# Kernel tuning notes

Measured on AMD Instinct MI355X. Metric: run time of the kernel, lower is better.

## Reference

```python
import jax, jax.numpy as jnp
import numpy as np

NB, D, ED, N, K, DTR = 4, 1024, 2048, 32, 4, 64
B, L = 1, 1024


def setup_inputs():
    key = jax.random.key(0)
    ks = jax.random.split(key, 10)
    g = lambda k, s, sc=0.02: jax.random.normal(k, s, dtype=jnp.float32) * sc
    A_log = jnp.log(jnp.broadcast_to(jnp.arange(1, N + 1, dtype=jnp.float32), (NB, ED, N))) + 0.0
    return {
        "x": g(ks[0], (B, L, D), 1.0),
        "Wi": g(ks[1], (D, D)),
        "bi": jnp.zeros((D,), jnp.float32),
        "ln_g": jnp.ones((NB, D), jnp.float32),
        "ln_b": jnp.zeros((NB, D), jnp.float32),
        "in_w": g(ks[2], (NB, 2 * ED, D)),
        "conv_w": g(ks[3], (NB, ED, 1, K), 0.2),
        "conv_b": jnp.zeros((NB, ED), jnp.float32),
        "xproj_w": g(ks[4], (NB, DTR + 2 * N, ED)),
        "dtproj_w": g(ks[5], (NB, ED, DTR), 0.1),
        "dtproj_b": jnp.full((NB, ED), -4.0, jnp.float32),
        "A_log": A_log,
        "Dp": jnp.ones((NB, ED), jnp.float32),
        "out_w": g(ks[6], (NB, D, ED)),
        "fn_g": jnp.ones((D,), jnp.float32),
        "fn_b": jnp.zeros((D,), jnp.float32),
        "sp_w": g(ks[7], (N, D)),
        "sp_b": jnp.zeros((N,), jnp.float32),
    }


def layernorm(x, g, b, eps=1e-5):
    m = jnp.mean(x, axis=-1, keepdims=True)
    v = jnp.mean(jnp.square(x - m), axis=-1, keepdims=True)
    return (x - m) * jax.lax.rsqrt(v + eps) * g + b


def mamba(u_in, in_w, conv_w, conv_b, xproj_w, dtproj_w, dtproj_b, A_log, Dp, out_w):
    # u_in: (B, L, D)
    xz = u_in @ in_w.T                       # (B, L, 2*ED)
    u, z = jnp.split(xz, 2, axis=-1)         # each (B, L, ED)
    # causal depthwise conv over time
    uc = jnp.swapaxes(u, 1, 2)               # (B, ED, L)
    uc = jax.lax.conv_general_dilated(uc, conv_w, (1,), [(K - 1, 0)], feature_group_count=ED)
    uc = uc + conv_b[None, :, None]
    u = jax.nn.silu(jnp.swapaxes(uc, 1, 2))  # (B, L, ED)
    x_dbl = u @ xproj_w.T                    # (B, L, DTR + 2N)
    dt, Bm, Cm = jnp.split(x_dbl, [DTR, DTR + N], axis=-1)
    delta = jax.nn.softplus(dt @ dtproj_w.T + dtproj_b)  # (B, L, ED)
    A = -jnp.exp(A_log)                                  # (ED, N)
    dA = jnp.exp(delta[..., None] * A)                   # (B, L, ED, N)
    dBu = (delta * u)[..., None] * Bm[:, :, None, :]     # (B, L, ED, N)

    def step(h, inp):
        dA_t, dBu_t, C_t = inp
        h = dA_t * h + dBu_t
        y = jnp.einsum('ben,bn->be', h, C_t)
        return h, y

    h0 = jnp.zeros((u.shape[0], ED, N), u.dtype)
    _, ys = jax.lax.scan(step, h0, (jnp.swapaxes(dA, 0, 1), jnp.swapaxes(dBu, 0, 1), jnp.swapaxes(Cm, 0, 1)))
    y = jnp.swapaxes(ys, 0, 1) + u * Dp      # (B, L, ED)
    y = y * jax.nn.silu(z)
    return y @ out_w.T                       # (B, L, D)


def reference(x, Wi, bi, ln_g, ln_b, in_w, conv_w, conv_b, xproj_w, dtproj_w, dtproj_b, A_log, Dp, out_w, fn_g, fn_b, sp_w, sp_b):
    h = x @ Wi.T + bi
    for i in range(NB):
        normed = layernorm(h, ln_g[i], ln_b[i])
        h = h + mamba(normed, in_w[i], conv_w[i], conv_b[i], xproj_w[i],
                      dtproj_w[i], dtproj_b[i], A_log[i], Dp[i], out_w[i])
    h = layernorm(h, fn_g, fn_b)
    state = jnp.mean(h, axis=1) @ sp_w.T + sp_b   # (B, N)
    return h, state
```

## Files before the change

kernel.cpp:

```cpp
#include <hip/hip_runtime.h>
#include <math.h>

#define D_    1024
#define ED_   2048
#define NST   32
#define KCONV 4
#define DTR_  64
#define L_    1024
#define NB_   4
#define NCH   8
#define CHUNK (L_ / NCH)
#define ZSPL  4
#define XPZ   16

typedef __bf16 bf16_8 __attribute__((ext_vector_type(8)));
typedef __bf16 bf16_4 __attribute__((ext_vector_type(4)));
typedef float  f32x4  __attribute__((ext_vector_type(4)));

__device__ __forceinline__ float softplus_f(float x) {
  return x > 20.f ? x : log1pf(expf(x));
}
__device__ __forceinline__ float silu_f(float x) {
  return x / (1.f + expf(-x));
}

__device__ __forceinline__ int xcd_swz(int lin, int nwg) {
  const int q = nwg >> 3;
  return (lin & 7) * q + (lin >> 3);
}

__global__ __launch_bounds__(256) void f2bf4_k(
    const float* __restrict__ i0, __bf16* __restrict__ o0, int n0,
    const float* __restrict__ i1, __bf16* __restrict__ o1, int n1,
    const float* __restrict__ i2, __bf16* __restrict__ o2, int n2,
    const float* __restrict__ i3, __bf16* __restrict__ o3, int n3)
{
  int gid = blockIdx.x * 256 + threadIdx.x;
  const int u0 = n0 >> 3, u1 = n1 >> 3, u2 = n2 >> 3, u3 = n3 >> 3;
  const float* in; __bf16* out;
  if (gid < u0) { in = i0; out = o0; }
  else if ((gid -= u0) < u1) { in = i1; out = o1; }
  else if ((gid -= u1) < u2) { in = i2; out = o2; }
  else if ((gid -= u2) < u3) { in = i3; out = o3; }
  else return;
  const int i = gid * 8;
  const float4 a = *reinterpret_cast<const float4*>(in + i);
  const float4 b = *reinterpret_cast<const float4*>(in + i + 4);
  bf16_8 v;
  v[0]=(__bf16)a.x; v[1]=(__bf16)a.y; v[2]=(__bf16)a.z; v[3]=(__bf16)a.w;
  v[4]=(__bf16)b.x; v[5]=(__bf16)b.y; v[6]=(__bf16)b.z; v[7]=(__bf16)b.w;
  *reinterpret_cast<bf16_8*>(out + i) = v;
}

__global__ __launch_bounds__(256) void gemm_mfma(
    const __bf16* __restrict__ A, int lda,
    const __bf16* __restrict__ W, int ldw,
    const float* __restrict__ bias, float* __restrict__ C, int ldc,
    int K, int flags)
{
  __shared__ __bf16 As[128 * 64];
  __shared__ __bf16 Ws[128 * 64];
  const int tid  = threadIdx.x;
  const int lane = tid & 63;
  const int w    = tid >> 6;
  const int wr   = w >> 1, wc = w & 1;
  const int nwg  = gridDim.x * gridDim.y;
  const int swz  = xcd_swz(blockIdx.y * gridDim.x + blockIdx.x, nwg);
  const int bx   = swz % gridDim.x, by = swz / gridDim.x;
  const int row0 = by * 128, col0 = bx * 128;

  f32x4 acc[4][4] = {};

  for (int k0 = 0; k0 < K; k0 += 64) {
    #pragma unroll
    for (int j = 0; j < 4; ++j) {
      const int inst = w * 4 + j;
      const int row  = inst * 8 + (lane >> 3);
      const int lu   = (lane & 7) ^ (row & 7);
      __builtin_amdgcn_global_load_lds(
          (const __attribute__((address_space(1))) void*)(A + (size_t)(row0 + row) * lda + k0 + lu * 8),
          (__attribute__((address_space(3))) void*)(&As[inst * 512]), 16, 0, 0);
      __builtin_amdgcn_global_load_lds(
          (const __attribute__((address_space(1))) void*)(W + (size_t)(col0 + row) * ldw + k0 + lu * 8),
          (__attribute__((address_space(3))) void*)(&Ws[inst * 512]), 16, 0, 0);
    }
    __syncthreads();
    const int r16 = lane & 15;
    const int uq  = lane >> 4;
    #pragma unroll
    for (int ks = 0; ks < 2; ++ks) {
      bf16_8 af[4], bfr[4];
      #pragma unroll
      for (int m = 0; m < 4; ++m) {
        const int row = wr * 64 + m * 16 + r16;
        const int pu  = (ks * 4 + uq) ^ (row & 7);
        af[m] = *reinterpret_cast<const bf16_8*>(&As[row * 64 + pu * 8]);
      }
      #pragma unroll
      for (int n = 0; n < 4; ++n) {
        const int row = wc * 64 + n * 16 + r16;
        const int pu  = (ks * 4 + uq) ^ (row & 7);
        bfr[n] = *reinterpret_cast<const bf16_8*>(&Ws[row * 64 + pu * 8]);
      }
      #pragma unroll
      for (int m = 0; m < 4; ++m)
        #pragma unroll
        for (int n = 0; n < 4; ++n)
          acc[m][n] = __builtin_amdgcn_mfma_f32_16x16x32_bf16(af[m], bfr[n], acc[m][n], 0, 0, 0);
    }
    __syncthreads();
  }

  const int crow = (lane >> 4) * 4;
  const int ccol = lane & 15;
  #pragma unroll
  for (int m = 0; m < 4; ++m)
    #pragma unroll
    for (int n = 0; n < 4; ++n) {
      const int col = col0 + wc * 64 + n * 16 + ccol;
      const float bv = (flags & 4) ? bias[col] : 0.f;
      #pragma unroll
      for (int r = 0; r < 4; ++r) {
        const int row = row0 + wr * 64 + m * 16 + crow + r;
        float* cp = C + (size_t)row * ldc + col;
        float v = acc[m][n][r] + bv;
        if (flags & 2) v = softplus_f(v);
        if (flags & 1) v += *cp;
        *cp = v;
      }
    }
}

__global__ __launch_bounds__(256) void gemm_mfma_sk(
    const __bf16* __restrict__ A, const __bf16* __restrict__ W,
    float* __restrict__ partials, int M, int N, int K, int Kc)
{
  __shared__ __bf16 As[128 * 64];
  __shared__ __bf16 Ws[128 * 64];
  const int tid  = threadIdx.x;
  const int lane = tid & 63;
  const int w    = tid >> 6;
  const int wr   = w >> 1, wc = w & 1;
  const int nwg  = gridDim.x * gridDim.y * gridDim.z;
  const int lin  = (blockIdx.z * gridDim.y + blockIdx.y) * gridDim.x + blockIdx.x;
  const int swz  = xcd_swz(lin, nwg);
  const int bx   = swz % gridDim.x;
  const int tmp  = swz / gridDim.x;
  const int by   = tmp % gridDim.y, bz = tmp / gridDim.y;
  const int row0 = by * 128, col0 = bx * 128;
  const int kbase = bz * Kc;

  f32x4 acc[4][4] = {};

  for (int k0 = kbase; k0 < kbase + Kc; k0 += 64) {
    #pragma unroll
    for (int j = 0; j < 4; ++j) {
      const int inst = w * 4 + j;
      const int row  = inst * 8 + (lane >> 3);
      const int lu   = (lane & 7) ^ (row & 7);
      __builtin_amdgcn_global_load_lds(
          (const __attribute__((address_space(1))) void*)(A + (size_t)(row0 + row) * K + k0 + lu * 8),
          (__attribute__((address_space(3))) void*)(&As[inst * 512]), 16, 0, 0);
      __builtin_amdgcn_global_load_lds(
          (const __attribute__((address_space(1))) void*)(W + (size_t)(col0 + row) * K + k0 + lu * 8),
          (__attribute__((address_space(3))) void*)(&Ws[inst * 512]), 16, 0, 0);
    }
    __syncthreads();
    const int r16 = lane & 15;
    const int uq  = lane >> 4;
    #pragma unroll
    for (int ks = 0; ks < 2; ++ks) {
      bf16_8 af[4], bfr[4];
      #pragma unroll
      for (int m = 0; m < 4; ++m) {
        const int row = wr * 64 + m * 16 + r16;
        const int pu  = (ks * 4 + uq) ^ (row & 7);
        af[m] = *reinterpret_cast<const bf16_8*>(&As[row * 64 + pu * 8]);
      }
      #pragma unroll
      for (int n = 0; n < 4; ++n) {
        const int row = wc * 64 + n * 16 + r16;
        const int pu  = (ks * 4 + uq) ^ (row & 7);
        bfr[n] = *reinterpret_cast<const bf16_8*>(&Ws[row * 64 + pu * 8]);
      }
      #pragma unroll
      for (int m = 0; m < 4; ++m)
        #pragma unroll
        for (int n = 0; n < 4; ++n)
          acc[m][n] = __builtin_amdgcn_mfma_f32_16x16x32_bf16(af[m], bfr[n], acc[m][n], 0, 0, 0);
    }
    __syncthreads();
  }

  float* base = partials + (size_t)bz * M * N;
  const int crow = (lane >> 4) * 4;
  const int ccol = lane & 15;
  #pragma unroll
  for (int m = 0; m < 4; ++m)
    #pragma unroll
    for (int n = 0; n < 4; ++n) {
      const int col = col0 + wc * 64 + n * 16 + ccol;
      #pragma unroll
      for (int r = 0; r < 4; ++r) {
        const int row = row0 + wr * 64 + m * 16 + crow + r;
        base[(size_t)row * N + col] = acc[m][n][r];
      }
    }
}

__global__ __launch_bounds__(256) void mfma_sk_reduce(
    const float* __restrict__ partials, const float* __restrict__ bias,
    float* __restrict__ C, __bf16* __restrict__ Cbf,
    int elems, int ncols, int nz, int flags)
{
  const int i = (blockIdx.x * 256 + threadIdx.x) * 4;
  if (i >= elems) return;
  float4 s = *reinterpret_cast<const float4*>(partials + i);
  for (int z = 1; z < nz; ++z) {
    const float4 p = *reinterpret_cast<const float4*>(partials + (size_t)z * elems + i);
    s.x += p.x; s.y += p.y; s.z += p.z; s.w += p.w;
  }
  if (flags & 4) {
    const float4 bv = *reinterpret_cast<const float4*>(bias + (i % ncols));
    s.x += bv.x; s.y += bv.y; s.z += bv.z; s.w += bv.w;
  }
  if (flags & 1) {
    const float4 ov = *reinterpret_cast<const float4*>(C + i);
    s.x += ov.x; s.y += ov.y; s.z += ov.z; s.w += ov.w;
  }
  *reinterpret_cast<float4*>(C + i) = s;
  if (flags & 8) {
    bf16_4 b;
    b[0]=(__bf16)s.x; b[1]=(__bf16)s.y; b[2]=(__bf16)s.z; b[3]=(__bf16)s.w;
    *reinterpret_cast<bf16_4*>(Cbf + i) = b;
  }
}

__global__ __launch_bounds__(256) void reduce_ln_k(
    const float* __restrict__ partials, const float* __restrict__ bias,
    float* __restrict__ hbuf, const float* __restrict__ g,
    const float* __restrict__ b, __bf16* __restrict__ outbf, int flags)
{
  __shared__ float red[8];
  const int row = blockIdx.x;
  const int tid = threadIdx.x;
  const int c = tid * 4;
  const size_t off = (size_t)row * D_ + c;
  float4 v = *reinterpret_cast<const float4*>(partials + off);
  #pragma unroll
  for (int z = 1; z < ZSPL; ++z) {
    const float4 p = *reinterpret_cast<const float4*>(partials + (size_t)z * (L_*D_) + off);
    v.x += p.x; v.y += p.y; v.z += p.z; v.w += p.w;
  }
  if (flags & 4) {
    const float4 bv = *reinterpret_cast<const float4*>(bias + c);
    v.x += bv.x; v.y += bv.y; v.z += bv.z; v.w += bv.w;
  }
  if (flags & 1) {
    const float4 ov = *reinterpret_cast<const float4*>(hbuf + off);
    v.x += ov.x; v.y += ov.y; v.z += ov.z; v.w += ov.w;
  }
  *reinterpret_cast<float4*>(hbuf + off) = v;

  float s = v.x + v.y + v.z + v.w;
  #pragma unroll
  for (int o = 32; o; o >>= 1) s += __shfl_down(s, o, 64);
  if ((tid & 63) == 0) red[tid >> 6] = s;
  __syncthreads();
  const float m = (red[0] + red[1] + red[2] + red[3]) * (1.f / D_);
  float dx0 = v.x - m, dx1 = v.y - m, dx2 = v.z - m, dx3 = v.w - m;
  float ss = dx0*dx0 + dx1*dx1 + dx2*dx2 + dx3*dx3;
  #pragma unroll
  for (int o = 32; o; o >>= 1) ss += __shfl_down(ss, o, 64);
  if ((tid & 63) == 0) red[4 + (tid >> 6)] = ss;
  __syncthreads();
  const float var = (red[4] + red[5] + red[6] + red[7]) * (1.f / D_);
  const float rs = rsqrtf(var + 1e-5f);
  const float4 gv = *reinterpret_cast<const float4*>(g + c);
  const float4 bv = *reinterpret_cast<const float4*>(b + c);
  bf16_4 o;
  o[0] = (__bf16)(dx0 * rs * gv.x + bv.x);
  o[1] = (__bf16)(dx1 * rs * gv.y + bv.y);
  o[2] = (__bf16)(dx2 * rs * gv.z + bv.z);
  o[3] = (__bf16)(dx3 * rs * gv.w + bv.w);
  *reinterpret_cast<bf16_4*>(outbf + off) = o;
}

__global__ __launch_bounds__(256) void layernorm_k(
    const float* __restrict__ x, const float* __restrict__ g,
    const float* __restrict__ b, float* __restrict__ out)
{
  __shared__ float red[8];
  const int row = blockIdx.x;
  const int tid = threadIdx.x;
  const float* xr = x + (size_t)row * D_;
  float4 v = *reinterpret_cast<const float4*>(xr + tid * 4);
  float s = v.x + v.y + v.z + v.w;
  #pragma unroll
  for (int off = 32; off; off >>= 1) s += __shfl_down(s, off, 64);
  if ((tid & 63) == 0) red[tid >> 6] = s;
  __syncthreads();
  const float m = (red[0] + red[1] + red[2] + red[3]) * (1.f / D_);
  float dx0 = v.x - m, dx1 = v.y - m, dx2 = v.z - m, dx3 = v.w - m;
  float ss = dx0*dx0 + dx1*dx1 + dx2*dx2 + dx3*dx3;
  #pragma unroll
  for (int off = 32; off; off >>= 1) ss += __shfl_down(ss, off, 64);
  if ((tid & 63) == 0) red[4 + (tid >> 6)] = ss;
  __syncthreads();
  const float var = (red[4] + red[5] + red[6] + red[7]) * (1.f / D_);
  const float rs = rsqrtf(var + 1e-5f);
  const int c = tid * 4;
  const float4 gv = *reinterpret_cast<const float4*>(g + c);
  const float4 bv = *reinterpret_cast<const float4*>(b + c);
  float4 o;
  o.x = dx0 * rs * gv.x + bv.x;
  o.y = dx1 * rs * gv.y + bv.y;
  o.z = dx2 * rs * gv.z + bv.z;
  o.w = dx3 * rs * gv.w + bv.w;
  *reinterpret_cast<float4*>(out + (size_t)row * D_ + c) = o;
}

__global__ __launch_bounds__(256) void conv_silu_k(
    const float* __restrict__ xz, const float* __restrict__ cw,
    const float* __restrict__ cb, float* __restrict__ u, __bf16* __restrict__ ub)
{
  const int e = blockIdx.x * 256 + threadIdx.x;
  const int t0 = blockIdx.y * 8;
  const float w0 = cw[e*4+0], w1 = cw[e*4+1], w2 = cw[e*4+2], w3 = cw[e*4+3];
  const float b = cb[e];
  float x0 = (t0 >= 3) ? xz[(size_t)(t0-3)*(2*ED_)+e] : 0.f;
  float x1 = (t0 >= 2) ? xz[(size_t)(t0-2)*(2*ED_)+e] : 0.f;
  float x2 = (t0 >= 1) ? xz[(size_t)(t0-1)*(2*ED_)+e] : 0.f;
  #pragma unroll
  for (int j = 0; j < 8; ++j) {
    const float x3 = xz[(size_t)(t0+j)*(2*ED_)+e];
    const float uv = silu_f(b + w0*x0 + w1*x1 + w2*x2 + w3*x3);
    u[(size_t)(t0+j)*ED_+e] = uv;
    ub[(size_t)(t0+j)*ED_+e] = (__bf16)uv;
    x0 = x1; x1 = x2; x2 = x3;
  }
}

__global__ __launch_bounds__(512) void scan_phase1(
    const float* __restrict__ delta, const float* __restrict__ u,
    const float* __restrict__ xdbl, const float* __restrict__ A_log,
    float* __restrict__ hend, float* __restrict__ Pend)
{
  __shared__ float dl[32][16], ul[32][16];
  __shared__ float bl[32][36];
  const int tid = threadIdx.x;
  const int n = tid & 31;
  const int c = tid >> 5;
  const int e0 = blockIdx.x * 16;
  const int e = e0 + c;
  const int ch = blockIdx.y;
  const float a = -expf(A_log[e * NST + n]);
  float h = 0.f, S = 0.f;
  const int t0 = ch * CHUNK;
  const int s_t = tid >> 4, s_e = tid & 15;
  const int b_t = tid >> 3, b_c = (tid & 7) * 4;

  float rg_d, rg_u;
  float4 rg_b;
  rg_d = delta[(size_t)(t0 + s_t) * ED_ + e0 + s_e];
  rg_u = u[(size_t)(t0 + s_t) * ED_ + e0 + s_e];
  if (tid < 256)
    rg_b = *reinterpret_cast<const float4*>(&xdbl[(size_t)(t0 + b_t) * 128 + 64 + b_c]);

  for (int tb = 0; tb < CHUNK; tb += 32) {
    dl[s_t][s_e] = rg_d;
    ul[s_t][s_e] = rg_u;
    if (tid < 256) *reinterpret_cast<float4*>(&bl[b_t][b_c]) = rg_b;
    __syncthreads();
    if (tb + 32 < CHUNK) {
      const int t = t0 + tb + 32 + s_t;
      rg_d = delta[(size_t)t * ED_ + e0 + s_e];
      rg_u = u[(size_t)t * ED_ + e0 + s_e];
      if (tid < 256)
        rg_b = *reinterpret_cast<const float4*>(&xdbl[(size_t)(t0 + tb + 32 + b_t) * 128 + 64 + b_c]);
    }
    #pragma unroll
    for (int jp = 0; jp < 16; ++jp) {
      const float sd1 = dl[2*jp][c],   uv1 = ul[2*jp][c],   B1 = bl[2*jp][n];
      const float sd2 = dl[2*jp+1][c], uv2 = ul[2*jp+1][c], B2 = bl[2*jp+1][n];
      const float dA1 = __expf(sd1 * a);
      const float dA2 = __expf(sd2 * a);
      const float b1 = sd1 * uv1 * B1;
      const float b2 = sd2 * uv2 * B2;
      h = fmaf(dA1 * dA2, h, fmaf(dA2, b1, b2));
      S += sd1 + sd2;
    }
    __syncthreads();
  }
  const int idx = ch * (ED_ * NST) + blockIdx.x * 512 + tid;
  hend[idx] = h;
  Pend[idx] = __expf(a * S);
}

__global__ __launch_bounds__(512) void scan_phase3(
    const float* __restrict__ delta, const float* __restrict__ u,
    const float* __restrict__ xdbl, const float* __restrict__ A_log,
    const float* __restrict__ hend, const float* __restrict__ Pend,
    const float* __restrict__ Dp,
    const float* __restrict__ xz, __bf16* __restrict__ y)
{
  __shared__ __bf16 p_lds[16][16][34];
  __shared__ float dl[16][16], ul[16][16], zl[16][16];
  __shared__ float bc[16][68];
  const int tid = threadIdx.x;
  const int n = tid & 31;
  const int c = tid >> 5;
  const int e0 = blockIdx.x * 16;
  const int e = e0 + c;
  const int ch = blockIdx.y;
  const float a = -expf(A_log[e * NST + n]);
  const float dp = Dp[e];

  float h = 0.f;
  {
    const int sidx = blockIdx.x * 512 + tid;
    for (int cc = 0; cc < ch; ++cc) {
      const int off = cc * (ED_ * NST) + sidx;
      h = fmaf(Pend[off], h, hend[off]);
    }
  }

  const int t0 = ch * CHUNK;
  const int r = n & 15, half = n >> 4;
  const int s_t  = (tid & 255) >> 4;
  const int s_e  = tid & 15;
  const int bidx = tid - 256;
  const int b_t  = (bidx & 255) >> 4;
  const int b_c  = (bidx & 15) * 4;

  float rg_a = 0.f, rg_z = 0.f;
  float4 rg_bc;
  {
    const int t = t0 + s_t;
    if (tid < 256) {
      rg_a = delta[(size_t)t * ED_ + e0 + s_e];
      rg_z = xz[(size_t)t * (2*ED_) + ED_ + e0 + s_e];
    } else {
      rg_a = u[(size_t)t * ED_ + e0 + s_e];
      rg_bc = *reinterpret_cast<const float4*>(&xdbl[(size_t)(t0 + b_t) * 128 + 64 + b_c]);
    }
  }

  for (int tb = 0; tb < CHUNK; tb += 16) {
    if (tid < 256) {
      dl[s_t][s_e] = rg_a; zl[s_t][s_e] = rg_z;
    } else {
      ul[s_t][s_e] = rg_a;
      *reinterpret_cast<float4*>(&bc[b_t][b_c]) = rg_bc;
    }
    __syncthreads();
    if (tb + 16 < CHUNK) {
      const int t = t0 + tb + 16 + s_t;
      if (tid < 256) {
        rg_a = delta[(size_t)t * ED_ + e0 + s_e];
        rg_z = xz[(size_t)t * (2*ED_) + ED_ + e0 + s_e];
      } else {
        rg_a = u[(size_t)t * ED_ + e0 + s_e];
        rg_bc = *reinterpret_cast<const float4*>(&xdbl[(size_t)(t0 + tb + 16 + b_t) * 128 + 64 + b_c]);
      }
    }
    #pragma unroll
    for (int jp = 0; jp < 8; ++jp) {
      const float sd1 = dl[2*jp][c],   uv1 = ul[2*jp][c];
      const float sd2 = dl[2*jp+1][c], uv2 = ul[2*jp+1][c];
      const float B1 = bc[2*jp][n],   C1 = bc[2*jp][32 + n];
      const float B2 = bc[2*jp+1][n], C2 = bc[2*jp+1][32 + n];
      const float dA1 = __expf(sd1 * a);
      const float dA2 = __expf(sd2 * a);
      const float b1 = sd1 * uv1 * B1;
      const float b2 = sd2 * uv2 * B2;
      const float h1 = fmaf(dA1, h, b1);
      p_lds[c][2*jp][n] = (__bf16)(h1 * C1);
      h = fmaf(dA1 * dA2, h, fmaf(dA2, b1, b2));
      p_lds[c][2*jp+1][n] = (__bf16)(h * C2);
    }
    __syncthreads();
    float s = 0.f;
    #pragma unroll
    for (int k = 0; k < 8; ++k) {
      const unsigned v = *reinterpret_cast<const unsigned*>(&p_lds[c][r][half * 16 + 2 * k]);
      s += __uint_as_float(v << 16) + __uint_as_float(v & 0xffff0000u);
    }
    s += __shfl_xor(s, 16, 64);
    if (half == 0) {
      const float uvt = ul[r][c];
      const float zv  = zl[r][c];
      y[(size_t)(t0 + tb + r) * ED_ + e] = (__bf16)((s + uvt * dp) * silu_f(zv));
    }
    __syncthreads();
  }
}

__global__ __launch_bounds__(256) void colmean_part_k(
    const float* __restrict__ hf, float* __restrict__ part)
{
  const int d = blockIdx.x * 256 + threadIdx.x;
  const int tc = blockIdx.y;
  float s = 0.f;
  #pragma unroll 8
  for (int j = 0; j < 32; ++j) s += hf[(size_t)(tc * 32 + j) * D_ + d];
  part[tc * D_ + d] = s;
}

__global__ __launch_bounds__(256) void state_fused_k(
    const float* __restrict__ part, const float* __restrict__ spw,
    const float* __restrict__ spb, float* __restrict__ out)
{
  __shared__ float red[4];
  const int nidx = blockIdx.x;
  const int tid = threadIdx.x;
  float s = 0.f;
  for (int d = tid; d < D_; d += 256) {
    float cm = 0.f;
    #pragma unroll
    for (int c = 0; c < 32; ++c) cm += part[c * D_ + d];
    s += cm * (1.f / L_) * spw[(size_t)nidx * D_ + d];
  }
  #pragma unroll
  for (int off = 32; off; off >>= 1) s += __shfl_down(s, off, 64);
  if ((tid & 63) == 0) red[tid >> 6] = s;
  __syncthreads();
  if (tid == 0) out[nidx] = red[0] + red[1] + red[2] + red[3] + spb[nidx];
}

extern "C" void kernel_launch(void* const* d_in, const int* in_sizes, int n_in,
                              void* d_out, int out_size, void* d_ws, size_t ws_size,
                              hipStream_t stream) {
  const float* x        = (const float*)d_in[0];
  const float* Wi       = (const float*)d_in[1];
  const float* bi       = (const float*)d_in[2];
  const float* ln_g     = (const float*)d_in[3];
  const float* ln_b     = (const float*)d_in[4];
  const float* in_w     = (const float*)d_in[5];
  const float* conv_w   = (const float*)d_in[6];
  const float* conv_b   = (const float*)d_in[7];
  const float* xproj_w  = (const float*)d_in[8];
  const float* dtproj_w = (const float*)d_in[9];
  const float* dtproj_b = (const float*)d_in[10];
  const float* A_log    = (const float*)d_in[11];
  const float* Dp       = (const float*)d_in[12];
  const float* out_w    = (const float*)d_in[13];
  const float* fn_g     = (const float*)d_in[14];
  const float* fn_b     = (const float*)d_in[15];
  const float* sp_w     = (const float*)d_in[16];
  const float* sp_b     = (const float*)d_in[17];
  float* out  = (float*)d_out;
  float* ws_f = (float*)d_ws;

  float* h_buf  = ws_f;
  float* xz     = ws_f + 1048576;
  float* u_buf  = ws_f + 5242880;
  float* xdbl   = ws_f + 7340032;
  float* delta  = ws_f + 7471104;
  float* hend   = ws_f + 9568256;
  float* pend   = ws_f + 10092544;
  __bf16* nbf   = (__bf16*)(ws_f + 10617856);
  __bf16* ybf   = (__bf16*)(ws_f + 11142144);
  __bf16* wbf   = (__bf16*)(ws_f + 12190720);
  __bf16* xdblbf= (__bf16*)(ws_f + 16385024);
  __bf16* dtwbf = (__bf16*)(ws_f + 16450560);
  __bf16* ubf   = (__bf16*)(ws_f + 16516096);
  __bf16* xpbf  = (__bf16*)(ws_f + 17564672);
  __bf16* owbf  = (__bf16*)(ws_f + 17695744);
  float* skmf   = u_buf;
  float* skxp   = delta;
  float* cmpart = hend;

  const dim3 blk(256);
  const dim3 blk512(512);

  f2bf4_k<<<1024, blk, 0, stream>>>(x, nbf, L_*D_, Wi, wbf, D_*D_,
                                    x, nbf, 0, x, nbf, 0);
  gemm_mfma_sk<<<dim3(D_/128, L_/128, ZSPL), blk, 0, stream>>>(
      nbf, wbf, skmf, L_, D_, D_, D_/ZSPL);
  reduce_ln_k<<<L_, blk, 0, stream>>>(
      skmf, bi, h_buf, ln_g, ln_b, nbf, 4);

  for (int i = 0; i < NB_; ++i) {
    f2bf4_k<<<3264, blk, 0, stream>>>(
        in_w    + (size_t)i*2*ED_*D_, wbf,   2*ED_*D_,
        xproj_w + (size_t)i*128*ED_,  xpbf,  128*ED_,
        dtproj_w+ (size_t)i*ED_*DTR_, dtwbf, ED_*DTR_,
        out_w   + (size_t)i*D_*ED_,   owbf,  D_*ED_);
    gemm_mfma<<<dim3(2*ED_/128, L_/128), blk, 0, stream>>>(
        nbf, D_, wbf, D_, nullptr, xz, 2*ED_, D_, 0);
    conv_silu_k<<<dim3(ED_/256, L_/8), blk, 0, stream>>>(
        xz, conv_w + (size_t)i*ED_*KCONV, conv_b + (size_t)i*ED_, u_buf, ubf);
    gemm_mfma_sk<<<dim3(1, L_/128, XPZ), blk, 0, stream>>>(
        ubf, xpbf, skxp, L_, 128, ED_, ED_/XPZ);
    mfma_sk_reduce<<<dim3(L_*128/4/256), blk, 0, stream>>>(
        skxp, nullptr, xdbl, xdblbf, L_*128, 128, XPZ, 8);
    gemm_mfma<<<dim3(ED_/128, L_/128), blk, 0, stream>>>(
        xdblbf, 128, dtwbf, DTR_, dtproj_b + (size_t)i*ED_, delta, ED_, DTR_, 2 | 4);
    scan_phase1<<<dim3(ED_/16, NCH), blk512, 0, stream>>>(
        delta, u_buf, xdbl, A_log + (size_t)i*ED_*NST, hend, pend);
    scan_phase3<<<dim3(ED_/16, NCH), blk512, 0, stream>>>(
        delta, u_buf, xdbl, A_log + (size_t)i*ED_*NST, hend, pend,
        Dp + (size_t)i*ED_, xz, ybf);
    gemm_mfma_sk<<<dim3(D_/128, L_/128, ZSPL), blk, 0, stream>>>(
        ybf, owbf, skmf, L_, D_, ED_, ED_/ZSPL);
    if (i < NB_ - 1) {
      reduce_ln_k<<<L_, blk, 0, stream>>>(
          skmf, nullptr, h_buf, ln_g + (i+1)*D_, ln_b + (i+1)*D_, nbf, 1);
    } else {
      mfma_sk_reduce<<<dim3(L_*D_/4/256), blk, 0, stream>>>(
          skmf, nullptr, h_buf, nullptr, L_*D_, D_, ZSPL, 1);
    }
  }

  layernorm_k<<<L_, blk, 0, stream>>>(h_buf, fn_g, fn_b, out);
  colmean_part_k<<<dim3(D_/256, 32), blk, 0, stream>>>(out, cmpart);
  state_fused_k<<<NST, blk, 0, stream>>>(cmpart, sp_w, sp_b, out + (size_t)L_*D_);
}
```

Before: 656.8 us.

## Store in_proj output and conv activations as bf16, drop fp32 u buffer

The in_proj GEMM gets a new flag that writes its xz output as bf16 instead of fp32. The conv, scan_phase1 and scan_phase3 kernels now read bf16 xz and u, and the fp32 u buffer is no longer written, which cuts global memory traffic between these stages. Separately, scan_phase3 keeps per-step partial products in fp32 shared memory instead of packed bf16, and it drops the trailing barrier by reading ul/zl before the mid-loop sync. The risks are lower precision in the z/u inputs to the scan and a subtle synchronisation change in scan_phase3.

```diff
diff --git a/kernel.cpp b/kernel.cpp
--- a/kernel.cpp
+++ b/kernel.cpp
@@ -113,6 +113,7 @@
 
   const int crow = (lane >> 4) * 4;
   const int ccol = lane & 15;
+  __bf16* Cb = reinterpret_cast<__bf16*>(C);
   #pragma unroll
   for (int m = 0; m < 4; ++m)
     #pragma unroll
@@ -122,11 +123,15 @@
       #pragma unroll
       for (int r = 0; r < 4; ++r) {
         const int row = row0 + wr * 64 + m * 16 + crow + r;
-        float* cp = C + (size_t)row * ldc + col;
         float v = acc[m][n][r] + bv;
         if (flags & 2) v = softplus_f(v);
-        if (flags & 1) v += *cp;
-        *cp = v;
+        if (flags & 8) {
+          Cb[(size_t)row * ldc + col] = (__bf16)v;
+        } else {
+          float* cp = C + (size_t)row * ldc + col;
+          if (flags & 1) v += *cp;
+          *cp = v;
+        }
       }
     }
 }
@@ -321,28 +326,27 @@
 }
 
 __global__ __launch_bounds__(256) void conv_silu_k(
-    const float* __restrict__ xz, const float* __restrict__ cw,
-    const float* __restrict__ cb, float* __restrict__ u, __bf16* __restrict__ ub)
+    const __bf16* __restrict__ xzb, const float* __restrict__ cw,
+    const float* __restrict__ cb, __bf16* __restrict__ ub)
 {
   const int e = blockIdx.x * 256 + threadIdx.x;
   const int t0 = blockIdx.y * 8;
   const float w0 = cw[e*4+0], w1 = cw[e*4+1], w2 = cw[e*4+2], w3 = cw[e*4+3];
   const float b = cb[e];
-  float x0 = (t0 >= 3) ? xz[(size_t)(t0-3)*(2*ED_)+e] : 0.f;
-  float x1 = (t0 >= 2) ? xz[(size_t)(t0-2)*(2*ED_)+e] : 0.f;
-  float x2 = (t0 >= 1) ? xz[(size_t)(t0-1)*(2*ED_)+e] : 0.f;
+  float x0 = (t0 >= 3) ? (float)xzb[(size_t)(t0-3)*(2*ED_)+e] : 0.f;
+  float x1 = (t0 >= 2) ? (float)xzb[(size_t)(t0-2)*(2*ED_)+e] : 0.f;
+  float x2 = (t0 >= 1) ? (float)xzb[(size_t)(t0-1)*(2*ED_)+e] : 0.f;
   #pragma unroll
   for (int j = 0; j < 8; ++j) {
-    const float x3 = xz[(size_t)(t0+j)*(2*ED_)+e];
+    const float x3 = (float)xzb[(size_t)(t0+j)*(2*ED_)+e];
     const float uv = silu_f(b + w0*x0 + w1*x1 + w2*x2 + w3*x3);
-    u[(size_t)(t0+j)*ED_+e] = uv;
     ub[(size_t)(t0+j)*ED_+e] = (__bf16)uv;
     x0 = x1; x1 = x2; x2 = x3;
   }
 }
 
 __global__ __launch_bounds__(512) void scan_phase1(
-    const float* __restrict__ delta, const float* __restrict__ u,
+    const float* __restrict__ delta, const __bf16* __restrict__ ub,
     const float* __restrict__ xdbl, const float* __restrict__ A_log,
     float* __restrict__ hend, float* __restrict__ Pend)
 {
@@ -363,7 +367,7 @@
   float rg_d, rg_u;
   float4 rg_b;
   rg_d = delta[(size_t)(t0 + s_t) * ED_ + e0 + s_e];
-  rg_u = u[(size_t)(t0 + s_t) * ED_ + e0 + s_e];
+  rg_u = (float)ub[(size_t)(t0 + s_t) * ED_ + e0 + s_e];
   if (tid < 256)
     rg_b = *reinterpret_cast<const float4*>(&xdbl[(size_t)(t0 + b_t) * 128 + 64 + b_c]);
 
@@ -375,7 +379,7 @@
     if (tb + 32 < CHUNK) {
       const int t = t0 + tb + 32 + s_t;
       rg_d = delta[(size_t)t * ED_ + e0 + s_e];
-      rg_u = u[(size_t)t * ED_ + e0 + s_e];
+      rg_u = (float)ub[(size_t)t * ED_ + e0 + s_e];
       if (tid < 256)
         rg_b = *reinterpret_cast<const float4*>(&xdbl[(size_t)(t0 + tb + 32 + b_t) * 128 + 64 + b_c]);
     }
@@ -398,13 +402,13 @@
 }
 
 __global__ __launch_bounds__(512) void scan_phase3(
-    const float* __restrict__ delta, const float* __restrict__ u,
+    const float* __restrict__ delta, const __bf16* __restrict__ ub,
     const float* __restrict__ xdbl, const float* __restrict__ A_log,
     const float* __restrict__ hend, const float* __restrict__ Pend,
     const float* __restrict__ Dp,
-    const float* __restrict__ xz, __bf16* __restrict__ y)
-{
-  __shared__ __bf16 p_lds[16][16][34];
+    const __bf16* __restrict__ xzb, __bf16* __restrict__ y)
+{
+  __shared__ float p_lds[16][16][33];
   __shared__ float dl[16][16], ul[16][16], zl[16][16];
   __shared__ float bc[16][68];
   const int tid = threadIdx.x;
@@ -439,9 +443,9 @@
     const int t = t0 + s_t;
     if (tid < 256) {
       rg_a = delta[(size_t)t * ED_ + e0 + s_e];
-      rg_z = xz[(size_t)t * (2*ED_) + ED_ + e0 + s_e];
+      rg_z = (float)xzb[(size_t)t * (2*ED_) + ED_ + e0 + s_e];
     } else {
-      rg_a = u[(size_t)t * ED_ + e0 + s_e];
+      rg_a = (float)ub[(size_t)t * ED_ + e0 + s_e];
       rg_bc = *reinterpret_cast<const float4*>(&xdbl[(size_t)(t0 + b_t) * 128 + 64 + b_c]);
     }
   }
@@ -458,9 +462,9 @@
       const int t = t0 + tb + 16 + s_t;
       if (tid < 256) {
         rg_a = delta[(size_t)t * ED_ + e0 + s_e];
-        rg_z = xz[(size_t)t * (2*ED_) + ED_ + e0 + s_e];
+        rg_z = (float)xzb[(size_t)t * (2*ED_) + ED_ + e0 + s_e];
       } else {
-        rg_a = u[(size_t)t * ED_ + e0 + s_e];
+        rg_a = (float)ub[(size_t)t * ED_ + e0 + s_e];
         rg_bc = *reinterpret_cast<const float4*>(&xdbl[(size_t)(t0 + tb + 16 + b_t) * 128 + 64 + b_c]);
       }
     }
@@ -475,24 +479,20 @@
       const float b1 = sd1 * uv1 * B1;
       const float b2 = sd2 * uv2 * B2;
       const float h1 = fmaf(dA1, h, b1);
-      p_lds[c][2*jp][n] = (__bf16)(h1 * C1);
+      p_lds[c][2*jp][n] = h1 * C1;
       h = fmaf(dA1 * dA2, h, fmaf(dA2, b1, b2));
-      p_lds[c][2*jp+1][n] = (__bf16)(h * C2);
-    }
+      p_lds[c][2*jp+1][n] = h * C2;
+    }
+    const float uvt = ul[r][c];
+    const float zv  = zl[r][c];
     __syncthreads();
     float s = 0.f;
     #pragma unroll
-    for (int k = 0; k < 8; ++k) {
-      const unsigned v = *reinterpret_cast<const unsigned*>(&p_lds[c][r][half * 16 + 2 * k]);
-      s += __uint_as_float(v << 16) + __uint_as_float(v & 0xffff0000u);
-    }
+    for (int k = 0; k < 16; ++k) s += p_lds[c][r][half * 16 + k];
     s += __shfl_xor(s, 16, 64);
     if (half == 0) {
-      const float uvt = ul[r][c];
-      const float zv  = zl[r][c];
       y[(size_t)(t0 + tb + r) * ED_ + e] = (__bf16)((s + uvt * dp) * silu_f(zv));
     }
-    __syncthreads();
   }
 }
 
@@ -567,6 +567,7 @@
   __bf16* ubf   = (__bf16*)(ws_f + 16516096);
   __bf16* xpbf  = (__bf16*)(ws_f + 17564672);
   __bf16* owbf  = (__bf16*)(ws_f + 17695744);
+  __bf16* xzb   = (__bf16*)xz;
   float* skmf   = u_buf;
   float* skxp   = delta;
   float* cmpart = hend;
@@ -588,9 +589,9 @@
         dtproj_w+ (size_t)i*ED_*DTR_, dtwbf, ED_*DTR_,
         out_w   + (size_t)i*D_*ED_,   owbf,  D_*ED_);
     gemm_mfma<<<dim3(2*ED_/128, L_/128), blk, 0, stream>>>(
-        nbf, D_, wbf, D_, nullptr, xz, 2*ED_, D_, 0);
+        nbf, D_, wbf, D_, nullptr, (float*)xzb, 2*ED_, D_, 8);
     conv_silu_k<<<dim3(ED_/256, L_/8), blk, 0, stream>>>(
-        xz, conv_w + (size_t)i*ED_*KCONV, conv_b + (size_t)i*ED_, u_buf, ubf);
+        xzb, conv_w + (size_t)i*ED_*KCONV, conv_b + (size_t)i*ED_, ubf);
     gemm_mfma_sk<<<dim3(1, L_/128, XPZ), blk, 0, stream>>>(
         ubf, xpbf, skxp, L_, 128, ED_, ED_/XPZ);
     mfma_sk_reduce<<<dim3(L_*128/4/256), blk, 0, stream>>>(
@@ -598,10 +599,10 @@
     gemm_mfma<<<dim3(ED_/128, L_/128), blk, 0, stream>>>(
         xdblbf, 128, dtwbf, DTR_, dtproj_b + (size_t)i*ED_, delta, ED_, DTR_, 2 | 4);
     scan_phase1<<<dim3(ED_/16, NCH), blk512, 0, stream>>>(
-        delta, u_buf, xdbl, A_log + (size_t)i*ED_*NST, hend, pend);
+        delta, ubf, xdbl, A_log + (size_t)i*ED_*NST, hend, pend);
     scan_phase3<<<dim3(ED_/16, NCH), blk512, 0, stream>>>(
-        delta, u_buf, xdbl, A_log + (size_t)i*ED_*NST, hend, pend,
-        Dp + (size_t)i*ED_, xz, ybf);
+        delta, ubf, xdbl, A_log + (size_t)i*ED_*NST, hend, pend,
+        Dp + (size_t)i*ED_, xzb, ybf);
     gemm_mfma_sk<<<dim3(D_/128, L_/128, ZSPL), blk, 0, stream>>>(
         ybf, owbf, skmf, L_, D_, ED_, ED_/ZSPL);
     if (i < NB_ - 1) {
```

New measurement: 691.5 us. +5.3%, slower.

## Shrink scan blocks to 256 threads and use fp32 partials in phase3

Applied to the files above, without the earlier changes.

Both scan kernels now cover 8 channels per block with 256 threads instead of 16 channels with 512 threads, doubling the grid, and scan_phase3 gets a launch bound of 7 blocks per CU. Phase3 stores h*C partials in fp32 LDS instead of packed bf16 and replaces the paired two-step recurrence with a plain per-step update. The aim is better occupancy and scheduling flexibility on the latency-bound scan. The cost is more blocks, duplicated B/C loads per block, and larger LDS per channel for the fp32 partials.

```diff
diff --git a/kernel.cpp b/kernel.cpp
--- a/kernel.cpp
+++ b/kernel.cpp
@@ -341,43 +341,41 @@
   }
 }
 
-__global__ __launch_bounds__(512) void scan_phase1(
+__global__ __launch_bounds__(256) void scan_phase1(
     const float* __restrict__ delta, const float* __restrict__ u,
     const float* __restrict__ xdbl, const float* __restrict__ A_log,
     float* __restrict__ hend, float* __restrict__ Pend)
 {
-  __shared__ float dl[32][16], ul[32][16];
-  __shared__ float bl[32][36];
+  __shared__ float dl[32][8], ul[32][8];
+  __shared__ float bl[32][32];
   const int tid = threadIdx.x;
   const int n = tid & 31;
   const int c = tid >> 5;
-  const int e0 = blockIdx.x * 16;
+  const int e0 = blockIdx.x * 8;
   const int e = e0 + c;
   const int ch = blockIdx.y;
   const float a = -expf(A_log[e * NST + n]);
   float h = 0.f, S = 0.f;
   const int t0 = ch * CHUNK;
-  const int s_t = tid >> 4, s_e = tid & 15;
+  const int s_t = tid >> 3, s_e = tid & 7;
   const int b_t = tid >> 3, b_c = (tid & 7) * 4;
 
   float rg_d, rg_u;
   float4 rg_b;
   rg_d = delta[(size_t)(t0 + s_t) * ED_ + e0 + s_e];
   rg_u = u[(size_t)(t0 + s_t) * ED_ + e0 + s_e];
-  if (tid < 256)
-    rg_b = *reinterpret_cast<const float4*>(&xdbl[(size_t)(t0 + b_t) * 128 + 64 + b_c]);
+  rg_b = *reinterpret_cast<const float4*>(&xdbl[(size_t)(t0 + b_t) * 128 + 64 + b_c]);
 
   for (int tb = 0; tb < CHUNK; tb += 32) {
     dl[s_t][s_e] = rg_d;
     ul[s_t][s_e] = rg_u;
-    if (tid < 256) *reinterpret_cast<float4*>(&bl[b_t][b_c]) = rg_b;
+    *reinterpret_cast<float4*>(&bl[b_t][b_c]) = rg_b;
     __syncthreads();
     if (tb + 32 < CHUNK) {
       const int t = t0 + tb + 32 + s_t;
       rg_d = delta[(size_t)t * ED_ + e0 + s_e];
       rg_u = u[(size_t)t * ED_ + e0 + s_e];
-      if (tid < 256)
-        rg_b = *reinterpret_cast<const float4*>(&xdbl[(size_t)(t0 + tb + 32 + b_t) * 128 + 64 + b_c]);
+      rg_b = *reinterpret_cast<const float4*>(&xdbl[(size_t)(t0 + tb + 32 + b_t) * 128 + 64 + b_c]);
     }
     #pragma unroll
     for (int jp = 0; jp < 16; ++jp) {
@@ -392,25 +390,25 @@
     }
     __syncthreads();
   }
-  const int idx = ch * (ED_ * NST) + blockIdx.x * 512 + tid;
+  const int idx = ch * (ED_ * NST) + blockIdx.x * 256 + tid;
   hend[idx] = h;
   Pend[idx] = __expf(a * S);
 }
 
-__global__ __launch_bounds__(512) void scan_phase3(
+__global__ __launch_bounds__(256, 7) void scan_phase3(
     const float* __restrict__ delta, const float* __restrict__ u,
     const float* __restrict__ xdbl, const float* __restrict__ A_log,
     const float* __restrict__ hend, const float* __restrict__ Pend,
     const float* __restrict__ Dp,
     const float* __restrict__ xz, __bf16* __restrict__ y)
 {
-  __shared__ __bf16 p_lds[16][16][34];
-  __shared__ float dl[16][16], ul[16][16], zl[16][16];
-  __shared__ float bc[16][68];
+  __shared__ float p_lds[8][16][33];
+  __shared__ float dl[16][8], ul[16][8], zl[16][8];
+  __shared__ float bc[16][64];
   const int tid = threadIdx.x;
   const int n = tid & 31;
   const int c = tid >> 5;
-  const int e0 = blockIdx.x * 16;
+  const int e0 = blockIdx.x * 8;
   const int e = e0 + c;
   const int ch = blockIdx.y;
   const float a = -expf(A_log[e * NST + n]);
@@ -418,7 +416,7 @@
 
   float h = 0.f;
   {
-    const int sidx = blockIdx.x * 512 + tid;
+    const int sidx = blockIdx.x * 256 + tid;
     for (int cc = 0; cc < ch; ++cc) {
       const int off = cc * (ED_ * NST) + sidx;
       h = fmaf(Pend[off], h, hend[off]);
@@ -427,65 +425,53 @@
 
   const int t0 = ch * CHUNK;
   const int r = n & 15, half = n >> 4;
-  const int s_t  = (tid & 255) >> 4;
-  const int s_e  = tid & 15;
-  const int bidx = tid - 256;
-  const int b_t  = (bidx & 255) >> 4;
-  const int b_c  = (bidx & 15) * 4;
+  const int s_t  = (tid & 127) >> 3;
+  const int s_e  = tid & 7;
+  const int b_t  = tid >> 4;
+  const int b_c  = (tid & 15) * 4;
 
   float rg_a = 0.f, rg_z = 0.f;
   float4 rg_bc;
   {
     const int t = t0 + s_t;
-    if (tid < 256) {
+    if (tid < 128) {
       rg_a = delta[(size_t)t * ED_ + e0 + s_e];
       rg_z = xz[(size_t)t * (2*ED_) + ED_ + e0 + s_e];
     } else {
       rg_a = u[(size_t)t * ED_ + e0 + s_e];
-      rg_bc = *reinterpret_cast<const float4*>(&xdbl[(size_t)(t0 + b_t) * 128 + 64 + b_c]);
-    }
+    }
+    rg_bc = *reinterpret_cast<const float4*>(&xdbl[(size_t)(t0 + b_t) * 128 + 64 + b_c]);
   }
 
   for (int tb = 0; tb < CHUNK; tb += 16) {
-    if (tid < 256) {
-      dl[s_t][s_e] = rg_a; zl[s_t][s_e] = rg_z;
-    } else {
-      ul[s_t][s_e] = rg_a;
-      *reinterpret_cast<float4*>(&bc[b_t][b_c]) = rg_bc;
-    }
+    if (tid < 128) { dl[s_t][s_e] = rg_a; zl[s_t][s_e] = rg_z; }
+    else          { ul[s_t][s_e] = rg_a; }
+    *reinterpret_cast<float4*>(&bc[b_t][b_c]) = rg_bc;
     __syncthreads();
     if (tb + 16 < CHUNK) {
       const int t = t0 + tb + 16 + s_t;
-      if (tid < 256) {
+      if (tid < 128) {
         rg_a = delta[(size_t)t * ED_ + e0 + s_e];
         rg_z = xz[(size_t)t * (2*ED_) + ED_ + e0 + s_e];
       } else {
         rg_a = u[(size_t)t * ED_ + e0 + s_e];
-        rg_bc = *reinterpret_cast<const float4*>(&xdbl[(size_t)(t0 + tb + 16 + b_t) * 128 + 64 + b_c]);
       }
-    }
-    #pragma unroll
-    for (int jp = 0; jp < 8; ++jp) {
-      const float sd1 = dl[2*jp][c],   uv1 = ul[2*jp][c];
-      const float sd2 = dl[2*jp+1][c], uv2 = ul[2*jp+1][c];
-      const float B1 = bc[2*jp][n],   C1 = bc[2*jp][32 + n];
-      const float B2 = bc[2*jp+1][n], C2 = bc[2*jp+1][32 + n];
-      const float dA1 = __expf(sd1 * a);
-      const float dA2 = __expf(sd2 * a);
-      const float b1 = sd1 * uv1 * B1;
-      const float b2 = sd2 * uv2 * B2;
-      const float h1 = fmaf(dA1, h, b1);
-      p_lds[c][2*jp][n] = (__bf16)(h1 * C1);
-      h = fmaf(dA1 * dA2, h, fmaf(dA2, b1, b2));
-      p_lds[c][2*jp+1][n] = (__bf16)(h * C2);
+      rg_bc = *reinterpret_cast<const float4*>(&xdbl[(size_t)(t0 + tb + 16 + b_t) * 128 + 64 + b_c]);
+    }
+    #pragma unroll
+    for (int j = 0; j < 16; ++j) {
+      const float sd = dl[j][c];
+      const float uv = ul[j][c];
+      const float Bv = bc[j][n];
+      const float Cv = bc[j][32 + n];
+      const float dA = __expf(sd * a);
+      h = fmaf(dA, h, sd * uv * Bv);
+      p_lds[c][j][n] = h * Cv;
     }
     __syncthreads();
     float s = 0.f;
     #pragma unroll
-    for (int k = 0; k < 8; ++k) {
-      const unsigned v = *reinterpret_cast<const unsigned*>(&p_lds[c][r][half * 16 + 2 * k]);
-      s += __uint_as_float(v << 16) + __uint_as_float(v & 0xffff0000u);
-    }
+    for (int k = 0; k < 16; ++k) s += p_lds[c][r][half * 16 + k];
     s += __shfl_xor(s, 16, 64);
     if (half == 0) {
       const float uvt = ul[r][c];
@@ -572,7 +558,6 @@
   float* cmpart = hend;
 
   const dim3 blk(256);
-  const dim3 blk512(512);
 
   f2bf4_k<<<1024, blk, 0, stream>>>(x, nbf, L_*D_, Wi, wbf, D_*D_,
                                     x, nbf, 0, x, nbf, 0);
@@ -597,9 +582,9 @@
         skxp, nullptr, xdbl, xdblbf, L_*128, 128, XPZ, 8);
     gemm_mfma<<<dim3(ED_/128, L_/128), blk, 0, stream>>>(
         xdblbf, 128, dtwbf, DTR_, dtproj_b + (size_t)i*ED_, delta, ED_, DTR_, 2 | 4);
-    scan_phase1<<<dim3(ED_/16, NCH), blk512, 0, stream>>>(
+    scan_phase1<<<dim3(ED_/8, NCH), blk, 0, stream>>>(
         delta, u_buf, xdbl, A_log + (size_t)i*ED_*NST, hend, pend);
-    scan_phase3<<<dim3(ED_/16, NCH), blk512, 0, stream>>>(
+    scan_phase3<<<dim3(ED_/8, NCH), blk, 0, stream>>>(
         delta, u_buf, xdbl, A_log + (size_t)i*ED_*NST, hend, pend,
         Dp + (size_t)i*ED_, xz, ybf);
     gemm_mfma_sk<<<dim3(D_/128, L_/128, ZSPL), blk, 0, stream>>>(
```

After: 651.0 us. About the same (-0.9%).
